# Optimization experiments

Hardware: AMD Instinct MI355X
Metric: run time of the kernel (lower is better)

Reference implementation:

```python
import jax, jax.numpy as jnp
import numpy as np

B, S, C, HD = 2, 1024, 1024, 64
H = C // HD  # 16 heads
E = 4
EPS = 1e-5


def _ln(x, g, b):
    m = jnp.mean(x, axis=-1, keepdims=True)
    v = jnp.mean(jnp.square(x - m), axis=-1, keepdims=True)
    return (x - m) / jnp.sqrt(v + EPS) * g + b


def setup_inputs() -> dict:
    key = jax.random.key(0)
    ks = jax.random.split(key, 16)
    s = 0.02
    return {
        "fwd_x": jax.random.normal(ks[0], (B, S + 1, C), jnp.float32),
        "bwd_x": jax.random.normal(ks[1], (B, S + 1, C), jnp.float32),
        "pos_embed": jax.random.normal(ks[2], (S, HD), jnp.float32) * 0.01,
        "ln1_g": jnp.ones((C,), jnp.float32),
        "ln1_b": jnp.zeros((C,), jnp.float32),
        "Wq": jax.random.normal(ks[3], (C, C), jnp.float32) * s,
        "bq": jnp.zeros((C,), jnp.float32),
        "Wk": jax.random.normal(ks[4], (C, C), jnp.float32) * s,
        "bk": jnp.zeros((C,), jnp.float32),
        "Wv": jax.random.normal(ks[5], (C, C), jnp.float32) * s,
        "bv": jnp.zeros((C,), jnp.float32),
        "Wo": jax.random.normal(ks[6], (C, C), jnp.float32) * s,
        "bo": jnp.zeros((C,), jnp.float32),
        "ln2_g": jnp.ones((C,), jnp.float32),
        "ln2_b": jnp.zeros((C,), jnp.float32),
        "mlp_g": jnp.ones((C,), jnp.float32),
        "mlp_b": jnp.zeros((C,), jnp.float32),
        "W1": jax.random.normal(ks[7], (C, E * C), jnp.float32) * s,
        "b1": jnp.zeros((E * C,), jnp.float32),
        "W2": jax.random.normal(ks[8], (E * C, C), jnp.float32) * s,
        "b2": jnp.zeros((C,), jnp.float32),
    }


def reference(fwd_x, bwd_x, pos_embed, ln1_g, ln1_b, Wq, bq, Wk, bk, Wv, bv,
              Wo, bo, ln2_g, ln2_b, mlp_g, mlp_b, W1, b1, W2, b2):
    f = fwd_x[:, :-1, :]   # [B, S, C]
    r = bwd_x[:, 1:, :]    # [B, S, C]
    comb = (f + r) * np.float32(1.0 / np.sqrt(2.0))

    all_embed = jnp.concatenate([f, r], axis=1)       # [B, 2S, C]
    cx = _ln(comb, ln1_g, ln1_b)
    ae = _ln(all_embed, ln1_g, ln1_b)

    q = (cx @ Wq + bq).reshape(B, S, H, HD)
    k = (ae @ Wk + bk).reshape(B, 2 * S, H, HD)
    v = (ae @ Wv + bv).reshape(B, 2 * S, H, HD)

    pos2 = jnp.concatenate([pos_embed, pos_embed], axis=0)  # [2S, HD]
    k = k + pos2[None, :, None, :]
    q = (q + pos_embed[None, :, None, :]) * np.float32(1.0 / np.sqrt(HD))

    logits = jnp.einsum('bqhd,bkhd->bhqk', q, k)      # [B, H, S, 2S]

    qi = jnp.arange(S)[:, None]
    ki = jnp.arange(S)[None, :]
    l2r = ki <= qi   # causal (keys up to and incl. q) on first half
    r2l = ki >= qi   # anti-causal on second half
    mask = jnp.concatenate([l2r, r2l], axis=-1)        # [S, 2S]

    neg = jnp.finfo(logits.dtype).min
    attn = jax.nn.softmax(jnp.where(mask[None, None], logits, neg), axis=-1)

    o = jnp.einsum('bhqk,bkhd->bqhd', attn, v).reshape(B, S, C)
    o = o @ Wo + bo

    x = comb + o
    h = _ln(_ln(x, ln2_g, ln2_b), mlp_g, mlp_b)
    m = jax.nn.gelu(h @ W1 + b1, approximate=False) @ W2 + b2
    return x + m
```

## Files before the change

kernel.cpp:

```cpp
#include <hip/hip_runtime.h>
#include <hip/hip_bf16.h>
#include <cstdint>

#define DI __device__ __forceinline__

typedef unsigned short u16;
typedef __bf16 bf16x8 __attribute__((ext_vector_type(8)));
typedef float f32x4 __attribute__((ext_vector_type(4)));

constexpr int Bc  = 2;
constexpr int Sc  = 1024;
constexpr int Cc  = 1024;
constexpr int Hc  = 16;
constexpr int HDc = 64;
constexpr int S2c = 2048;
constexpr int ECc = 4096;
constexpr int BSc  = Bc * Sc;
constexpr int BS2c = Bc * S2c;

constexpr int EPI_KV = 0, EPI_Q = 1, EPI_O = 3, EPI_GELU = 4, EPI_FINAL = 5;

DI u16 f2b(float f) {
  __hip_bfloat16 h = __float2bfloat16(f);
  u16 u;
  __builtin_memcpy(&u, &h, 2);
  return u;
}

DI u16 f2b_fast(float f) {
  uint32_t u;
  __builtin_memcpy(&u, &f, 4);
  return (u16)((u + 0x8000u) >> 16);
}

DI void glds16(const void* g, void* l) {
  auto* lp = reinterpret_cast<__attribute__((address_space(3))) uint32_t*>(
      reinterpret_cast<uintptr_t>(l));
  __builtin_amdgcn_global_load_lds(
      reinterpret_cast<const __attribute__((address_space(1))) uint32_t*>(
          reinterpret_cast<uintptr_t>(g)),
      lp, 16, 0, 0);
}

DI f32x4 mfma16(bf16x8 a, bf16x8 b, f32x4 c) {
  return __builtin_amdgcn_mfma_f32_16x16x32_bf16(a, b, c, 0, 0, 0);
}

#define PIPE_WAIT(N)                                            \
  do {                                                          \
    asm volatile("s_waitcnt vmcnt(" #N ")" ::: "memory");       \
    __builtin_amdgcn_sched_barrier(0);                          \
  } while (0)
#define PIPE_BAR()                                              \
  do {                                                          \
    __builtin_amdgcn_s_barrier();                               \
    __builtin_amdgcn_sched_barrier(0);                          \
  } while (0)
#define LGKM_FENCE()                                            \
  do {                                                          \
    asm volatile("s_waitcnt lgkmcnt(0)" ::: "memory");          \
    __builtin_amdgcn_sched_barrier(0);                          \
  } while (0)

__global__ __launch_bounds__(256) void transpose4_kernel(const float* __restrict__ Wq,
                                                         const float* __restrict__ Wk,
                                                         const float* __restrict__ Wv,
                                                         const float* __restrict__ Wo,
                                                         u16* __restrict__ WqT,
                                                         u16* __restrict__ WkvT,
                                                         u16* __restrict__ WoT) {
  __shared__ float tile[32][33];
  const int z = blockIdx.z;
  const float* W = (z == 0) ? Wq : (z == 1) ? Wk : (z == 2) ? Wv : Wo;
  u16* WT = (z == 0) ? WqT : (z == 1) ? WkvT : (z == 2) ? (WkvT + (size_t)Cc * Cc) : WoT;
  const int bx = blockIdx.x, by = blockIdx.y;
  const int tx = threadIdx.x, ty = threadIdx.y;
  const int c = bx * 32 + tx;
#pragma unroll
  for (int i = ty; i < 32; i += 8) tile[i][tx] = W[(size_t)(by * 32 + i) * Cc + c];
  __syncthreads();
#pragma unroll
  for (int i = ty; i < 32; i += 8)
    WT[(size_t)(bx * 32 + i) * Cc + by * 32 + tx] = f2b(tile[tx][i]);
}

__global__ __launch_bounds__(256) void transpose_kernel(const float* __restrict__ W,
                                                        u16* __restrict__ WT, int R, int Cn) {
  __shared__ float tile[32][33];
  const int bx = blockIdx.x, by = blockIdx.y;
  const int tx = threadIdx.x, ty = threadIdx.y;
  const int c = bx * 32 + tx;
#pragma unroll
  for (int i = ty; i < 32; i += 8) tile[i][tx] = W[(size_t)(by * 32 + i) * Cn + c];
  __syncthreads();
#pragma unroll
  for (int i = ty; i < 32; i += 8)
    WT[(size_t)(bx * 32 + i) * R + by * 32 + tx] = f2b(tile[tx][i]);
}

__global__ __launch_bounds__(256) void prep_ln_kernel(
    const float* __restrict__ fwd, const float* __restrict__ bwd, const float* __restrict__ g,
    const float* __restrict__ be, float* __restrict__ comb, u16* __restrict__ cx,
    u16* __restrict__ ae) {
  __shared__ float red[2][4];
  const int row = blockIdx.x, tid = threadIdx.x;
  const int c = tid * 4;
  float4 x;
  u16* dst;
  if (row < BSc) {
    const int b = row >> 10, s = row & (Sc - 1);
    const float4 f = *(const float4*)(fwd + ((size_t)(b * (Sc + 1) + s)) * Cc + c);
    const float4 r = *(const float4*)(bwd + ((size_t)(b * (Sc + 1) + s + 1)) * Cc + c);
    const float k = 0.70710678118654752f;
    x.x = (f.x + r.x) * k; x.y = (f.y + r.y) * k;
    x.z = (f.z + r.z) * k; x.w = (f.w + r.w) * k;
    *(float4*)(comb + (size_t)row * Cc + c) = x;
    dst = cx + (size_t)row * Cc;
  } else {
    const int idx = row - BSc;
    const int b = idx >> 11, t = idx & (S2c - 1);
    const float* src = (t < Sc) ? (fwd + ((size_t)(b * (Sc + 1) + t)) * Cc)
                                : (bwd + ((size_t)(b * (Sc + 1) + (t - Sc) + 1)) * Cc);
    x = *(const float4*)(src + c);
    dst = ae + (size_t)idx * Cc;
  }
  float s1 = x.x + x.y + x.z + x.w;
  float s2 = x.x * x.x + x.y * x.y + x.z * x.z + x.w * x.w;
  for (int off = 32; off; off >>= 1) { s1 += __shfl_down(s1, off); s2 += __shfl_down(s2, off); }
  if ((tid & 63) == 0) { red[0][tid >> 6] = s1; red[1][tid >> 6] = s2; }
  __syncthreads();
  s1 = red[0][0] + red[0][1] + red[0][2] + red[0][3];
  s2 = red[1][0] + red[1][1] + red[1][2] + red[1][3];
  const float mean = s1 * (1.0f / Cc);
  const float rstd = rsqrtf(s2 * (1.0f / Cc) - mean * mean + 1e-5f);
  const float4 gv = *(const float4*)(g + c);
  const float4 bv = *(const float4*)(be + c);
  ushort4 o;
  o.x = f2b((x.x - mean) * rstd * gv.x + bv.x);
  o.y = f2b((x.y - mean) * rstd * gv.y + bv.y);
  o.z = f2b((x.z - mean) * rstd * gv.z + bv.z);
  o.w = f2b((x.w - mean) * rstd * gv.w + bv.w);
  *(ushort4*)(dst + c) = o;
}

__global__ __launch_bounds__(256) void ln2_kernel(const float* __restrict__ x,
                                                  const float* __restrict__ g2,
                                                  const float* __restrict__ b2,
                                                  const float* __restrict__ gm,
                                                  const float* __restrict__ bm,
                                                  u16* __restrict__ h) {
  __shared__ float red[2][4];
  const int row = blockIdx.x, tid = threadIdx.x;
  const int c = tid * 4;
  const float4 v = *(const float4*)(x + (size_t)row * Cc + c);
  float s1 = v.x + v.y + v.z + v.w;
  float s2 = v.x * v.x + v.y * v.y + v.z * v.z + v.w * v.w;
  for (int off = 32; off; off >>= 1) { s1 += __shfl_down(s1, off); s2 += __shfl_down(s2, off); }
  if ((tid & 63) == 0) { red[0][tid >> 6] = s1; red[1][tid >> 6] = s2; }
  __syncthreads();
  s1 = red[0][0] + red[0][1] + red[0][2] + red[0][3];
  s2 = red[1][0] + red[1][1] + red[1][2] + red[1][3];
  float mean = s1 * (1.0f / Cc);
  float rstd = rsqrtf(s2 * (1.0f / Cc) - mean * mean + 1e-5f);
  const float4 ga = *(const float4*)(g2 + c);
  const float4 ba = *(const float4*)(b2 + c);
  const float t0 = (v.x - mean) * rstd * ga.x + ba.x;
  const float t1 = (v.y - mean) * rstd * ga.y + ba.y;
  const float t2 = (v.z - mean) * rstd * ga.z + ba.z;
  const float t3 = (v.w - mean) * rstd * ga.w + ba.w;
  s1 = t0 + t1 + t2 + t3;
  s2 = t0 * t0 + t1 * t1 + t2 * t2 + t3 * t3;
  for (int off = 32; off; off >>= 1) { s1 += __shfl_down(s1, off); s2 += __shfl_down(s2, off); }
  __syncthreads();
  if ((tid & 63) == 0) { red[0][tid >> 6] = s1; red[1][tid >> 6] = s2; }
  __syncthreads();
  s1 = red[0][0] + red[0][1] + red[0][2] + red[0][3];
  s2 = red[1][0] + red[1][1] + red[1][2] + red[1][3];
  mean = s1 * (1.0f / Cc);
  rstd = rsqrtf(s2 * (1.0f / Cc) - mean * mean + 1e-5f);
  const float4 gb = *(const float4*)(gm + c);
  const float4 bb = *(const float4*)(bm + c);
  ushort4 o;
  o.x = f2b((t0 - mean) * rstd * gb.x + bb.x);
  o.y = f2b((t1 - mean) * rstd * gb.y + bb.y);
  o.z = f2b((t2 - mean) * rstd * gb.z + bb.z);
  o.w = f2b((t3 - mean) * rstd * gb.w + bb.w);
  *(ushort4*)(h + (size_t)row * Cc + c) = o;
}

template <int EPI>
__global__ __launch_bounds__(512) void gemm_kernel(
    const u16* __restrict__ A, const u16* __restrict__ BT, const float* __restrict__ bias,
    const float* __restrict__ bias2, const float* __restrict__ pos,
    u16* __restrict__ outb, u16* __restrict__ out2, int M, int N, int K) {
  __shared__ u16 A0s[128 * 32], A1s[128 * 32], A2s[128 * 32], A3s[128 * 32];
  __shared__ u16 B0s[128 * 32], B1s[128 * 32], B2s[128 * 32], B3s[128 * 32];
  const int tid = threadIdx.x;
  const int w = tid >> 6, lane = tid & 63, quad = lane >> 4, r16 = lane & 15;
  const int bm = blockIdx.y * 128, bn = blockIdx.x * 128;
  const int wm = (w >> 2) * 64, wn = (w & 3) * 32;

  const int srow = tid >> 2, scol = (tid & 3) * 8;
  const u16* aP = A + (size_t)(bm + srow) * K + scol;
  const u16* bP = BT + (size_t)(bn + srow) * K + scol;
  const int stg = (w * 16) * 32;

  f32x4 acc[4][2] = {};

  auto STAGE = [&](u16* Ad, u16* Bd, int t) {
    const int ko = t * 32;
    glds16(aP + ko, Ad + stg);
    glds16(bP + ko, Bd + stg);
  };
  auto COMPUTE = [&](const u16* As, const u16* Bs) {
    bf16x8 af[4], bfr[2];
#pragma unroll
    for (int i = 0; i < 4; i++)
      af[i] = *reinterpret_cast<const bf16x8*>(&As[(wm + i * 16 + r16) * 32 + quad * 8]);
#pragma unroll
    for (int i = 0; i < 2; i++)
      bfr[i] = *reinterpret_cast<const bf16x8*>(&Bs[(wn + i * 16 + r16) * 32 + quad * 8]);
#pragma unroll
    for (int mi = 0; mi < 4; mi++)
#pragma unroll
      for (int ni = 0; ni < 2; ni++) acc[mi][ni] = mfma16(af[mi], bfr[ni], acc[mi][ni]);
  };

  const int NT = K / 32;
  STAGE(A0s, B0s, 0);
  STAGE(A1s, B1s, 1);
  for (int t = 0; t < NT; t += 4) {
    if (t + 2 < NT) { STAGE(A2s, B2s, t + 2); PIPE_WAIT(4); }
    else if (t + 1 < NT) PIPE_WAIT(2);
    else PIPE_WAIT(0);
    PIPE_BAR();
    COMPUTE(A0s, B0s);
    if (t + 3 < NT) { STAGE(A3s, B3s, t + 3); PIPE_WAIT(4); }
    else if (t + 2 < NT) PIPE_WAIT(2);
    else PIPE_WAIT(0);
    PIPE_BAR();
    COMPUTE(A1s, B1s);
    if (t + 4 < NT) { STAGE(A0s, B0s, t + 4); PIPE_WAIT(4); }
    else if (t + 3 < NT) PIPE_WAIT(2);
    else PIPE_WAIT(0);
    PIPE_BAR();
    COMPUTE(A2s, B2s);
    if (t + 5 < NT) { STAGE(A1s, B1s, t + 5); PIPE_WAIT(4); }
    else if (t + 4 < NT) PIPE_WAIT(2);
    else PIPE_WAIT(0);
    PIPE_BAR();
    COMPUTE(A3s, B3s);
  }

#pragma unroll
  for (int mi = 0; mi < 4; mi++) {
#pragma unroll
    for (int ni = 0; ni < 2; ni++) {
      const int col = bn + wn + ni * 16 + r16;
      const int row0 = bm + wm + mi * 16 + quad * 4;
      if constexpr (EPI == EPI_KV) {
        if (col < Cc) {
#pragma unroll
          for (int r = 0; r < 4; r++) {
            const int row = row0 + r;
            const int key = row & (S2c - 1);
            const float y =
                acc[mi][ni][r] + bias[col] + pos[(key & (Sc - 1)) * HDc + (col & 63)];
            outb[(size_t)row * Cc + col] = f2b(y);
          }
        } else {
          const int c2 = col - Cc;
          const int h = c2 >> 6, d = c2 & 63;
          const int b = row0 >> 11, key0 = row0 & (S2c - 1);
          const float bb = bias2[c2];
          ushort4 pk;
          pk.x = f2b(acc[mi][ni][0] + bb);
          pk.y = f2b(acc[mi][ni][1] + bb);
          pk.z = f2b(acc[mi][ni][2] + bb);
          pk.w = f2b(acc[mi][ni][3] + bb);
          *(ushort4*)&out2[(((size_t)(b * Hc + h) * HDc + d) << 11) + key0] = pk;
        }
      } else {
#pragma unroll
        for (int r = 0; r < 4; r++) {
          const float y = acc[mi][ni][r] + bias[col];
          outb[(size_t)(row0 + r) * N + col] =
              f2b(0.5f * y * (1.0f + erff(y * 0.70710678118654752f)));
        }
      }
    }
  }
}

template <int EPI>
__global__ __launch_bounds__(512) void gemm64_kernel(
    const u16* __restrict__ A, const u16* __restrict__ BT, const float* __restrict__ bias,
    const float* __restrict__ pos, const float* __restrict__ addsrc,
    u16* __restrict__ outb, float* __restrict__ outf, int M, int N, int K) {
  __shared__ u16 A0s[128 * 32], A1s[128 * 32], A2s[128 * 32], A3s[128 * 32];
  __shared__ u16 B0s[128 * 32], B1s[128 * 32], B2s[128 * 32], B3s[128 * 32];
  const int tid = threadIdx.x;
  const int w = tid >> 6, lane = tid & 63, quad = lane >> 4, r16 = lane & 15;
  const int kh = w >> 2, qd = w & 3;
  const int wm = (qd >> 1) * 32, wn = (qd & 1) * 32;
  const int bid = blockIdx.y * gridDim.x + blockIdx.x;
  const int swz = (bid & 7) * 64 + (bid >> 3);
  const int bx = swz & (gridDim.x - 1), by = swz / gridDim.x;
  const int bm = by * 64, bn = bx * 64;
  const int K2 = K >> 1;

  const int sr = (tid >> 2) & 63, sh = tid >> 8, scb = (tid & 3) * 8;
  const u16* aP = A + (size_t)(bm + sr) * K + sh * K2 + scb;
  const u16* bP = BT + (size_t)(bn + sr) * K + sh * K2 + scb;
  const int stg = w * 512;

  f32x4 acc[2][2] = {};

  auto STAGE = [&](u16* Ad, u16* Bd, int t) {
    glds16(aP + t * 32, Ad + stg);
    glds16(bP + t * 32, Bd + stg);
  };
  auto COMPUTE = [&](const u16* As, const u16* Bs) {
    bf16x8 af[2], bfr[2];
#pragma unroll
    for (int i = 0; i < 2; i++) {
      af[i] = *reinterpret_cast<const bf16x8*>(
          &As[(kh * 64 + wm + i * 16 + r16) * 32 + quad * 8]);
      bfr[i] = *reinterpret_cast<const bf16x8*>(
          &Bs[(kh * 64 + wn + i * 16 + r16) * 32 + quad * 8]);
    }
#pragma unroll
    for (int mi = 0; mi < 2; mi++)
#pragma unroll
      for (int ni = 0; ni < 2; ni++) acc[mi][ni] = mfma16(af[mi], bfr[ni], acc[mi][ni]);
  };

  const int NT = K2 / 32;
  STAGE(A0s, B0s, 0);
  STAGE(A1s, B1s, 1);
  for (int t = 0; t < NT; t += 4) {
    if (t + 2 < NT) { STAGE(A2s, B2s, t + 2); PIPE_WAIT(4); }
    else if (t + 1 < NT) PIPE_WAIT(2);
    else PIPE_WAIT(0);
    PIPE_BAR();
    COMPUTE(A0s, B0s);
    if (t + 3 < NT) { STAGE(A3s, B3s, t + 3); PIPE_WAIT(4); }
    else if (t + 2 < NT) PIPE_WAIT(2);
    else PIPE_WAIT(0);
    PIPE_BAR();
    COMPUTE(A1s, B1s);
    if (t + 4 < NT) { STAGE(A0s, B0s, t + 4); PIPE_WAIT(4); }
    else if (t + 3 < NT) PIPE_WAIT(2);
    else PIPE_WAIT(0);
    PIPE_BAR();
    COMPUTE(A2s, B2s);
    if (t + 5 < NT) { STAGE(A1s, B1s, t + 5); PIPE_WAIT(4); }
    else if (t + 4 < NT) PIPE_WAIT(2);
    else PIPE_WAIT(0);
    PIPE_BAR();
    COMPUTE(A3s, B3s);
  }

  PIPE_BAR();
  float* rb = (qd < 2 ? (float*)A0s : (float*)A1s) + (qd & 1) * 1024;
  if (kh == 1) {
#pragma unroll
    for (int mi = 0; mi < 2; mi++)
#pragma unroll
      for (int ni = 0; ni < 2; ni++)
#pragma unroll
        for (int r = 0; r < 4; r++)
          rb[(mi * 16 + quad * 4 + r) * 32 + ni * 16 + r16] = acc[mi][ni][r];
  }
  LGKM_FENCE();
  PIPE_BAR();
  if (kh == 0) {
#pragma unroll
    for (int mi = 0; mi < 2; mi++)
#pragma unroll
      for (int ni = 0; ni < 2; ni++) {
        const int col = bn + wn + ni * 16 + r16;
        const float bcol = bias[col];
#pragma unroll
        for (int r = 0; r < 4; r++) {
          const int row = bm + wm + mi * 16 + quad * 4 + r;
          const float y =
              acc[mi][ni][r] + rb[(mi * 16 + quad * 4 + r) * 32 + ni * 16 + r16] + bcol;
          const size_t flat = (size_t)row * N + col;
          if constexpr (EPI == EPI_Q) {
            constexpr float scq = 0.180336880111120426f;
            outb[flat] = f2b((y + pos[(row & (Sc - 1)) * HDc + (col & 63)]) * scq);
          } else {
            outf[flat] = y + addsrc[flat];
          }
        }
      }
  }
}

__global__ __launch_bounds__(256) void attn_kernel(const u16* __restrict__ qb,
                                                   const u16* __restrict__ kb,
                                                   const u16* __restrict__ vT,
                                                   u16* __restrict__ ob) {
  const int bh = blockIdx.x;
  const int qt = blockIdx.y;
  const int b = bh >> 4, head = bh & 15;
  const int tid = threadIdx.x;
  const int w = tid >> 6, lane = tid & 63, quad = lane >> 4, r16 = lane & 15;

  __shared__ u16 K0s[4096], K1s[4096], K2s[4096], K3s[4096];
  __shared__ u16 V0s[4096], V1s[4096], V2s[4096], V3s[4096];
  __shared__ u16 Ps[4][16 * 68];
  u16* ps = Ps[w];

  const int qw = qt * 64 + w * 16;

  bf16x8 aq[2];
  {
    const u16* qp = qb + ((size_t)((b * Sc + qw + r16) * Hc + head)) * HDc + quad * 8;
    aq[0] = *(const bf16x8*)qp;
    aq[1] = *(const bf16x8*)(qp + 32);
  }

  const size_t krow = (size_t)Hc * HDc;
  const u16* kbase = kb + ((size_t)b * S2c * Hc + head) * HDc;
  const u16* vbase = vT + ((size_t)(b * Hc + head)) * HDc * S2c;

  const int srow = w * 16 + (lane >> 2);
  const int scol = (lane & 3) * 8;
  const int stg = w * 16 * 32;
  const u16* kS = kbase + (size_t)srow * krow + scol;
  const u16* vS = vbase + (size_t)srow * S2c + scol;

  f32x4 o_acc[4] = {};
  float lsum[4] = {};

  auto K0OF = [&](int p) -> int { return (p <= qt) ? p * 64 : Sc + (p - 1) * 64; };

  auto STAGE = [&](u16* Kd, u16* Vd, int p) {
    const int k0 = K0OF(p);
    glds16(kS + (size_t)k0 * krow, Kd + stg);
    glds16(kS + (size_t)k0 * krow + 32, Kd + 2048 + stg);
    glds16(vS + k0, Vd + stg);
    glds16(vS + k0 + 32, Vd + 2048 + stg);
  };

  auto COMPUTE = [&](const u16* Kc, const u16* Vc, int p) {
    const int k0 = K0OF(p);
    f32x4 sacc[4] = {};
#pragma unroll
    for (int ks = 0; ks < 2; ks++)
#pragma unroll
      for (int ni = 0; ni < 4; ni++) {
        const bf16x8 bk = *(const bf16x8*)&Kc[ks * 2048 + (ni * 16 + r16) * 32 + quad * 8];
        sacc[ni] = mfma16(aq[ks], bk, sacc[ni]);
      }
    const int mode = (p == qt) ? 1 : ((p == qt + 1) ? 2 : 0);
#pragma unroll
    for (int r = 0; r < 4; r++) {
      const int qrow = qw + quad * 4 + r;
#pragma unroll
      for (int ni = 0; ni < 4; ni++) {
        float s = sacc[ni][r];
        if (mode == 1) { const int key = k0 + ni * 16 + r16; if (key > qrow) s = -128.0f; }
        else if (mode == 2) { const int key = k0 - Sc + ni * 16 + r16; if (key < qrow) s = -128.0f; }
        const float pe = __builtin_amdgcn_exp2f(s);
        lsum[r] += pe;
        ps[(quad * 4 + r) * 68 + ni * 16 + r16] = f2b_fast(pe);
      }
    }
#pragma unroll
    for (int ks = 0; ks < 2; ks++) {
      const bf16x8 ap = *(const bf16x8*)(&ps[r16 * 68 + ks * 32 + quad * 8]);
#pragma unroll
      for (int ni = 0; ni < 4; ni++) {
        const bf16x8 bv_ = *(const bf16x8*)&Vc[ks * 2048 + (ni * 16 + r16) * 32 + quad * 8];
        o_acc[ni] = mfma16(ap, bv_, o_acc[ni]);
      }
    }
  };

  constexpr int NU = 17;
  STAGE(K0s, V0s, 0);
  STAGE(K1s, V1s, 1);
  for (int t = 0; t < NU; t += 4) {
    {
      if (t + 2 < NU) { STAGE(K2s, V2s, t + 2); PIPE_WAIT(8); }
      else if (t + 1 < NU) PIPE_WAIT(4);
      else PIPE_WAIT(0);
      PIPE_BAR();
      COMPUTE(K0s, V0s, t);
    }
    if (t + 1 < NU) {
      if (t + 3 < NU) { STAGE(K3s, V3s, t + 3); PIPE_WAIT(8); }
      else if (t + 2 < NU) PIPE_WAIT(4);
      else PIPE_WAIT(0);
      PIPE_BAR();
      COMPUTE(K1s, V1s, t + 1);
    }
    if (t + 2 < NU) {
      if (t + 4 < NU) { STAGE(K0s, V0s, t + 4); PIPE_WAIT(8); }
      else if (t + 3 < NU) PIPE_WAIT(4);
      else PIPE_WAIT(0);
      PIPE_BAR();
      COMPUTE(K2s, V2s, t + 2);
    }
    if (t + 3 < NU) {
      if (t + 5 < NU) { STAGE(K1s, V1s, t + 5); PIPE_WAIT(8); }
      else if (t + 4 < NU) PIPE_WAIT(4);
      else PIPE_WAIT(0);
      PIPE_BAR();
      COMPUTE(K3s, V3s, t + 3);
    }
  }

#pragma unroll
  for (int r = 0; r < 4; r++) {
    float l = lsum[r];
    l += __shfl_xor(l, 1);
    l += __shfl_xor(l, 2);
    l += __shfl_xor(l, 4);
    l += __shfl_xor(l, 8);
    lsum[r] = 1.0f / l;
  }
#pragma unroll
  for (int r = 0; r < 4; r++) {
    u16* od = ob + ((size_t)((b * Sc + qw + quad * 4 + r) * Hc + head)) * HDc;
#pragma unroll
    for (int ni = 0; ni < 4; ni++) od[ni * 16 + r16] = f2b(o_acc[ni][r] * lsum[r]);
  }
}

extern "C" void kernel_launch(void* const* d_in, const int* in_sizes, int n_in, void* d_out,
                              int out_size, void* d_ws, size_t ws_size, hipStream_t stream) {
  const float* fwd = (const float*)d_in[0];
  const float* bwd = (const float*)d_in[1];
  const float* pos = (const float*)d_in[2];
  const float* ln1g = (const float*)d_in[3];
  const float* ln1b = (const float*)d_in[4];
  const float* Wq = (const float*)d_in[5];
  const float* bq = (const float*)d_in[6];
  const float* Wk = (const float*)d_in[7];
  const float* bk = (const float*)d_in[8];
  const float* Wv = (const float*)d_in[9];
  const float* bv = (const float*)d_in[10];
  const float* Wo = (const float*)d_in[11];
  const float* bo = (const float*)d_in[12];
  const float* ln2g = (const float*)d_in[13];
  const float* ln2b = (const float*)d_in[14];
  const float* mlpg = (const float*)d_in[15];
  const float* mlpb = (const float*)d_in[16];
  const float* W1 = (const float*)d_in[17];
  const float* b1 = (const float*)d_in[18];
  const float* W2 = (const float*)d_in[19];
  const float* b2 = (const float*)d_in[20];

  char* p = (char*)d_ws;
  auto alloc = [&](size_t bytes) -> char* {
    char* r = p;
    p += (bytes + 255) & ~(size_t)255;
    return r;
  };
  float* comb = (float*)alloc((size_t)BSc * Cc * 4);
  float* xbuf = (float*)alloc((size_t)BSc * Cc * 4);
  u16* cx = (u16*)alloc((size_t)BSc * Cc * 2);
  u16* ae = (u16*)alloc((size_t)BS2c * Cc * 2);
  u16* qbuf = (u16*)alloc((size_t)BSc * Cc * 2);
  u16* kbuf = (u16*)alloc((size_t)BS2c * Cc * 2);
  u16* vTb = (u16*)alloc((size_t)BS2c * Cc * 2);
  u16* obuf = (u16*)alloc((size_t)BSc * Cc * 2);
  u16* hb = (u16*)alloc((size_t)BSc * Cc * 2);
  u16* midb = (u16*)alloc((size_t)BSc * ECc * 2);
  u16* WqT = (u16*)alloc((size_t)Cc * Cc * 2);
  u16* WkvT = (u16*)alloc((size_t)2 * Cc * Cc * 2);
  u16* WoT = (u16*)alloc((size_t)Cc * Cc * 2);
  u16* W1T = (u16*)alloc((size_t)ECc * Cc * 2);
  u16* W2T = (u16*)alloc((size_t)Cc * ECc * 2);

  const dim3 tb(32, 8);
  transpose4_kernel<<<dim3(32, 32, 4), tb, 0, stream>>>(Wq, Wk, Wv, Wo, WqT, WkvT, WoT);
  transpose_kernel<<<dim3(128, 32), tb, 0, stream>>>(W1, W1T, Cc, ECc);
  transpose_kernel<<<dim3(32, 128), tb, 0, stream>>>(W2, W2T, ECc, Cc);

  prep_ln_kernel<<<BSc + BS2c, 256, 0, stream>>>(fwd, bwd, ln1g, ln1b, comb, cx, ae);

  gemm64_kernel<EPI_Q><<<dim3(Cc / 64, BSc / 64), 512, 0, stream>>>(
      cx, WqT, bq, pos, nullptr, qbuf, nullptr, BSc, Cc, Cc);

  gemm_kernel<EPI_KV><<<dim3(2 * Cc / 128, BS2c / 128), 512, 0, stream>>>(
      ae, WkvT, bk, bv, pos, kbuf, vTb, BS2c, 2 * Cc, Cc);

  attn_kernel<<<dim3(Bc * Hc, Sc / 64), 256, 0, stream>>>(qbuf, kbuf, vTb, obuf);

  gemm64_kernel<EPI_O><<<dim3(Cc / 64, BSc / 64), 512, 0, stream>>>(
      obuf, WoT, bo, nullptr, comb, nullptr, xbuf, BSc, Cc, Cc);

  ln2_kernel<<<BSc, 256, 0, stream>>>(xbuf, ln2g, ln2b, mlpg, mlpb, hb);

  gemm_kernel<EPI_GELU><<<dim3(ECc / 128, BSc / 128), 512, 0, stream>>>(
      hb, W1T, b1, nullptr, nullptr, midb, nullptr, BSc, ECc, Cc);

  gemm64_kernel<EPI_FINAL><<<dim3(Cc / 64, BSc / 64), 512, 0, stream>>>(
      midb, W2T, b2, nullptr, xbuf, nullptr, (float*)d_out, BSc, Cc, ECc);
}
```

Before: 300.2 us.

## Stage LDS tiles in MFMA fragment order to remove bank conflicts

Remaps the global-to-LDS staging thread mapping in both GEMM kernels and the attention kernel. Each 16x32 tile is now stored in the exact order a wave reads its MFMA fragments, so every lane reads a contiguous 16-byte chunk at lane*8. This is meant to remove LDS bank conflicts on the fragment reads, which previously used a row stride of 32 elements. In exchange, global load coalescing changes: each group of 16 lanes now reads 16 rows at the same 16-byte column rather than full 64-byte row segments.

```diff
diff --git a/kernel.cpp b/kernel.cpp
--- a/kernel.cpp
+++ b/kernel.cpp
@@ -200,10 +200,14 @@
   const int bm = blockIdx.y * 128, bn = blockIdx.x * 128;
   const int wm = (w >> 2) * 64, wn = (w & 3) * 32;
 
-  const int srow = tid >> 2, scol = (tid & 3) * 8;
+  const int srow = (tid >> 6) * 16 + (tid & 15);
+  const int scol = ((tid >> 4) & 3) * 8;
   const u16* aP = A + (size_t)(bm + srow) * K + scol;
   const u16* bP = BT + (size_t)(bn + srow) * K + scol;
   const int stg = (w * 16) * 32;
+
+  const int aoff = (wm >> 4) * 512 + lane * 8;
+  const int boff = (wn >> 4) * 512 + lane * 8;
 
   f32x4 acc[4][2] = {};
 
@@ -216,10 +220,10 @@
     bf16x8 af[4], bfr[2];
 #pragma unroll
     for (int i = 0; i < 4; i++)
-      af[i] = *reinterpret_cast<const bf16x8*>(&As[(wm + i * 16 + r16) * 32 + quad * 8]);
+      af[i] = *reinterpret_cast<const bf16x8*>(&As[aoff + i * 512]);
 #pragma unroll
     for (int i = 0; i < 2; i++)
-      bfr[i] = *reinterpret_cast<const bf16x8*>(&Bs[(wn + i * 16 + r16) * 32 + quad * 8]);
+      bfr[i] = *reinterpret_cast<const bf16x8*>(&Bs[boff + i * 512]);
 #pragma unroll
     for (int mi = 0; mi < 4; mi++)
 #pragma unroll
@@ -309,10 +313,15 @@
   const int bm = by * 64, bn = bx * 64;
   const int K2 = K >> 1;
 
-  const int sr = (tid >> 2) & 63, sh = tid >> 8, scb = (tid & 3) * 8;
+  const int br = (tid >> 6) * 16 + (tid & 15);
+  const int sr = br & 63, sh = br >> 6;
+  const int scb = ((tid >> 4) & 3) * 8;
   const u16* aP = A + (size_t)(bm + sr) * K + sh * K2 + scb;
   const u16* bP = BT + (size_t)(bn + sr) * K + sh * K2 + scb;
   const int stg = w * 512;
+
+  const int aoff = (kh * 4 + (wm >> 4)) * 512 + lane * 8;
+  const int boff = (kh * 4 + (wn >> 4)) * 512 + lane * 8;
 
   f32x4 acc[2][2] = {};
 
@@ -324,10 +333,8 @@
     bf16x8 af[2], bfr[2];
 #pragma unroll
     for (int i = 0; i < 2; i++) {
-      af[i] = *reinterpret_cast<const bf16x8*>(
-          &As[(kh * 64 + wm + i * 16 + r16) * 32 + quad * 8]);
-      bfr[i] = *reinterpret_cast<const bf16x8*>(
-          &Bs[(kh * 64 + wn + i * 16 + r16) * 32 + quad * 8]);
+      af[i] = *reinterpret_cast<const bf16x8*>(&As[aoff + i * 512]);
+      bfr[i] = *reinterpret_cast<const bf16x8*>(&Bs[boff + i * 512]);
     }
 #pragma unroll
     for (int mi = 0; mi < 2; mi++)
@@ -426,9 +433,9 @@
   const u16* kbase = kb + ((size_t)b * S2c * Hc + head) * HDc;
   const u16* vbase = vT + ((size_t)(b * Hc + head)) * HDc * S2c;
 
-  const int srow = w * 16 + (lane >> 2);
-  const int scol = (lane & 3) * 8;
-  const int stg = w * 16 * 32;
+  const int srow = w * 16 + (lane & 15);
+  const int scol = ((lane >> 4) & 3) * 8;
+  const int stg = w * 512;
   const u16* kS = kbase + (size_t)srow * krow + scol;
   const u16* vS = vbase + (size_t)srow * S2c + scol;
 
@@ -452,7 +459,7 @@
     for (int ks = 0; ks < 2; ks++)
 #pragma unroll
       for (int ni = 0; ni < 4; ni++) {
-        const bf16x8 bk = *(const bf16x8*)&Kc[ks * 2048 + (ni * 16 + r16) * 32 + quad * 8];
+        const bf16x8 bk = *(const bf16x8*)&Kc[ks * 2048 + ni * 512 + lane * 8];
         sacc[ni] = mfma16(aq[ks], bk, sacc[ni]);
       }
     const int mode = (p == qt) ? 1 : ((p == qt + 1) ? 2 : 0);
@@ -474,7 +481,7 @@
       const bf16x8 ap = *(const bf16x8*)(&ps[r16 * 68 + ks * 32 + quad * 8]);
 #pragma unroll
       for (int ni = 0; ni < 4; ni++) {
-        const bf16x8 bv_ = *(const bf16x8*)&Vc[ks * 2048 + (ni * 16 + r16) * 32 + quad * 8];
+        const bf16x8 bv_ = *(const bf16x8*)&Vc[ks * 2048 + ni * 512 + lane * 8];
         o_acc[ni] = mfma16(ap, bv_, o_acc[ni]);
       }
     }
```

Measured after the change: 360.4 us. 1.2x slower.
